# Kernel tuning notes

Measured on AMD Instinct MI355X. Metric: run time of the kernel, lower is better.

Reference implementation:

```python
import jax, jax.numpy as jnp
import numpy as np
import math

N = 8192
IN_FEATURES = 512
OUT_FEATURES = 512
BUCKET = 4          # self.bucket -> number of hash buckets
NHASH = 1           # nHashTable hardcoded to 1 in forward
NEG = -9e15         # sentinel used by the original module


def setup_inputs() -> dict:
    key = jax.random.key(0)
    k_in, k_adj, k_rot, k_kw, k_vw = jax.random.split(key, 5)
    inp = jax.random.normal(k_in, (N, IN_FEATURES), dtype=jnp.float32)
    adj = jax.random.randint(k_adj, (N, N), 0, 2, dtype=jnp.int32)
    rotations_rands = jax.random.normal(k_rot, (NHASH, OUT_FEATURES, BUCKET // 2), dtype=jnp.float32)
    # xavier_uniform with gain=1.414 for (in, out) matrices
    limit = 1.414 * math.sqrt(6.0 / (IN_FEATURES + OUT_FEATURES))
    kW = jax.random.uniform(k_kw, (IN_FEATURES, OUT_FEATURES), minval=-limit, maxval=limit, dtype=jnp.float32)
    vW = jax.random.uniform(k_vw, (IN_FEATURES, OUT_FEATURES), minval=-limit, maxval=limit, dtype=jnp.float32)
    return {"input": inp, "adj": adj, "rotations_rands": rotations_rands, "kW": kW, "vW": vW}


def reference(input, adj, rotations_rands, kW, vW):
    kh = input @ kW                      # [N, H]
    vh = input @ vW                      # [N, H]
    H = kh.shape[1]

    # LSH bucketing: rotate keys, argmax over [r, -r] -> bucket id per node
    rv = jnp.einsum('nh,thb->tnb', kh, rotations_rands)   # [1, N, B/2]
    rv = jnp.concatenate([rv, -rv], axis=-1)              # [1, N, B]
    buckets = jnp.argmax(rv, axis=2)[0]                   # [N]

    # Original scatters per-bucket kh@kh.T blocks into a dense NxN matrix
    # initialized at NEG; equivalent to masking full scores by same-bucket.
    same_bucket = buckets[:, None] == buckets[None, :]    # [N, N]
    scores = (kh @ kh.T) / jnp.sqrt(jnp.asarray(H, kh.dtype))
    K = jnp.where(same_bucket, scores, NEG)

    attention = jnp.where(adj > 0, K, NEG)
    attention = jax.nn.softmax(attention, axis=1)
    # dropout is identity in eval mode (reference runs in eval)
    h_prime = attention @ vh                              # [N, H]
    return jax.nn.elu(h_prime)                            # concat=True -> ELU
```

## Files before the change

kernel.cpp:

```cpp
#include <hip/hip_runtime.h>
#include <hip/hip_bf16.h>
#include <math.h>

#define N_NODES 8192
#define FEAT 512
#define NEGV -9e15f
#define VHPT_W 8704

typedef __attribute__((ext_vector_type(8))) short short8;
typedef __attribute__((ext_vector_type(4))) float floatx4;

#define OFF_VHP   16777216UL
#define OFF_KHP   33554432UL
#define OFF_VHPT  42074112UL
#define OFF_MASK  50987008UL
#define OFF_S     59375616UL
#define OFF_PERM  109707264UL
#define OFF_BUCK  109772800UL
#define OFF_META  109805568UL
#define OFF_CMEAN 109806592UL
#define OFF_ROWI  109841408UL
#define OFF_IPERM 109874176UL
#define WS_NEEDED 109906944UL
#define CAP_S     25165824L

#define OFF_AB    (OFF_S)
#define OFF_WKT   (OFF_S + 16777216UL)
#define OFF_WVT   (OFF_S + 17825792UL)
#define OFF_CW    (OFF_MASK)

static __device__ __forceinline__ unsigned short f2bf_bits(float x) {
  __hip_bfloat16 h = __float2bfloat16(x);
  unsigned short u;
  __builtin_memcpy(&u, &h, 2);
  return u;
}
static __device__ __forceinline__ float bf_bits2f(unsigned short u) {
  __hip_bfloat16 h;
  __builtin_memcpy(&h, &u, 2);
  return __bfloat162float(h);
}

static __device__ __forceinline__ void async_copy16(const void* gptr,
                                                    void* lptr) {
  __builtin_amdgcn_global_load_lds(
      (const __attribute__((address_space(1))) unsigned int*)gptr,
      (__attribute__((address_space(3))) unsigned int*)lptr, 16, 0, 0);
}

__global__ __launch_bounds__(256) void convert_input(
    const float* __restrict__ A, __hip_bfloat16* __restrict__ Ab) {
  const long idx = ((long)blockIdx.x * 256 + threadIdx.x) * 8;
  const float4 v0 = *(const float4*)&A[idx];
  const float4 v1 = *(const float4*)&A[idx + 4];
  const float vv[8] = {v0.x, v0.y, v0.z, v0.w, v1.x, v1.y, v1.z, v1.w};
  union { short8 s; unsigned short u[8]; } o;
#pragma unroll
  for (int e = 0; e < 8; e++) o.u[e] = f2bf_bits(vv[e]);
  *(short8*)&Ab[idx] = o.s;
}

__global__ __launch_bounds__(256) void convert_w(
    const float* __restrict__ kW, const float* __restrict__ vW,
    __hip_bfloat16* __restrict__ WkT, __hip_bfloat16* __restrict__ WvT) {
  __shared__ float tile[64][65];
  const int z = blockIdx.z;
  const float* __restrict__ W = z ? vW : kW;
  __hip_bfloat16* __restrict__ T = z ? WvT : WkT;
  const int k0 = blockIdx.x * 64, n0 = blockIdx.y * 64;
  const int t = threadIdx.x;
#pragma unroll
  for (int s = 0; s < 16; s++) {
    int idx = t + s * 256;
    int r = idx >> 6, c = idx & 63;
    tile[r][c] = W[(long)(k0 + r) * FEAT + n0 + c];
  }
  __syncthreads();
#pragma unroll
  for (int s = 0; s < 16; s++) {
    int idx = t + s * 256;
    int a = idx >> 6, b = idx & 63;
    unsigned short h = f2bf_bits(tile[b][a]);
    __builtin_memcpy(&T[(long)(n0 + a) * FEAT + k0 + b], &h, 2);
  }
}

__global__ __launch_bounds__(256) void mfma_dual(
    const __hip_bfloat16* __restrict__ Ab, const __hip_bfloat16* __restrict__ WkT,
    const __hip_bfloat16* __restrict__ WvT, const int* __restrict__ iperm,
    const int* __restrict__ meta, __hip_bfloat16* __restrict__ khp,
    __hip_bfloat16* __restrict__ vhp) {
  const int z = blockIdx.z;
  const __hip_bfloat16* __restrict__ WT = z ? WvT : WkT;
  const int ti = blockIdx.x, tj = blockIdx.y;
  __shared__ __align__(16) __hip_bfloat16 smem[32768];
  __hip_bfloat16* As = smem;
  __hip_bfloat16* Ws = smem + 16384;
  const int t = threadIdx.x;
  const int lane = t & 63, w = t >> 6;
  const int wm = (w >> 1) * 64, wn = (w & 1) * 64;
  const int quad = lane >> 4, ln = lane & 15;
  const int qr = quad * 8;
  floatx4 acc[4][4];
#pragma unroll
  for (int mi = 0; mi < 4; mi++)
#pragma unroll
    for (int ni = 0; ni < 4; ni++) acc[mi][ni] = (floatx4)0.f;

  auto STAGE = [&](int st, int buf) {
    const int k0 = st * 64;
#pragma unroll
    for (int p = 0; p < 2; p++)
#pragma unroll
      for (int s = 0; s < 2; s++) {
        int c = t + s * 256;
        int row = c >> 2, off8 = (c & 3) * 8;
        int lo = buf * 8192 + p * 4096 + row * 32 + off8;
        async_copy16(&Ab[(long)(ti * 128 + row) * FEAT + k0 + p * 32 + off8],
                     &As[lo]);
        async_copy16(&WT[(long)(tj * 128 + row) * FEAT + k0 + p * 32 + off8],
                     &Ws[lo]);
      }
  };
  STAGE(0, 0);
  __syncthreads();
  for (int st = 0; st < 8; st++) {
    const int buf = st & 1;
    if (st < 7) STAGE(st + 1, buf ^ 1);
#pragma unroll
    for (int p = 0; p < 2; p++) {
      short8 af[4], bfr[4];
#pragma unroll
      for (int mi = 0; mi < 4; mi++)
        af[mi] = *(const short8*)&As[buf * 8192 + p * 4096 +
                                     (wm + mi * 16 + ln) * 32 + qr];
#pragma unroll
      for (int ni = 0; ni < 4; ni++)
        bfr[ni] = *(const short8*)&Ws[buf * 8192 + p * 4096 +
                                      (wn + ni * 16 + ln) * 32 + qr];
#pragma unroll
      for (int mi = 0; mi < 4; mi++)
#pragma unroll
        for (int ni = 0; ni < 4; ni++)
          acc[mi][ni] = __builtin_amdgcn_mfma_f32_16x16x32_bf16(
              af[mi], bfr[ni], acc[mi][ni], 0, 0, 0);
    }
    __syncthreads();
  }
  __hip_bfloat16* Ct = smem;
#pragma unroll
  for (int mi = 0; mi < 4; mi++)
#pragma unroll
    for (int ni = 0; ni < 4; ni++) {
      int col = wn + ni * 16 + ln;
#pragma unroll
      for (int reg = 0; reg < 4; reg++) {
        int row = wm + mi * 16 + quad * 4 + reg;
        Ct[row * 136 + col] = __float2bfloat16(acc[mi][ni][reg]);
      }
    }
  __syncthreads();
  __hip_bfloat16* __restrict__ dst = z ? vhp : khp;
#pragma unroll
  for (int i = 0; i < 8; i++) {
    int idx = t + i * 256;
    int rl = idx >> 4, c8 = (idx & 15) * 8;
    int g = iperm[ti * 128 + rl];
    long drow = g;
    if (z) {
      int bb = (g >= meta[1]) + (g >= meta[2]) + (g >= meta[3]);
      drow = meta[14 + bb] + g - meta[bb];
    }
    *(short8*)&dst[drow * FEAT + tj * 128 + c8] =
        *(const short8*)&Ct[rl * 136 + c8];
  }
}

__global__ __launch_bounds__(64) void cw_kernel(
    const float* __restrict__ kW, const float* __restrict__ rot,
    double* __restrict__ cw) {
  const int f = blockIdx.x;
  const int lane = threadIdx.x;
  double r0 = 0.0, r1 = 0.0;
  for (int h = lane; h < FEAT; h += 64) {
    double a = (double)kW[(long)f * FEAT + h];
    r0 += a * (double)rot[2 * h];
    r1 += a * (double)rot[2 * h + 1];
  }
#pragma unroll
  for (int off = 32; off > 0; off >>= 1) {
    r0 += __shfl_down(r0, off);
    r1 += __shfl_down(r1, off);
  }
  if (lane == 0) {
    cw[2 * f] = r0;
    cw[2 * f + 1] = r1;
  }
}

__global__ __launch_bounds__(64) void rv_bucket_kernel(
    const float* __restrict__ input, const double* __restrict__ cw,
    int* __restrict__ buckets) {
  const int i = blockIdx.x;
  const int lane = threadIdx.x;
  double r0 = 0.0, r1 = 0.0;
  for (int f = lane; f < FEAT; f += 64) {
    double a = (double)input[(long)i * FEAT + f];
    r0 += a * cw[2 * f];
    r1 += a * cw[2 * f + 1];
  }
#pragma unroll
  for (int off = 32; off > 0; off >>= 1) {
    r0 += __shfl_down(r0, off);
    r1 += __shfl_down(r1, off);
  }
  if (lane == 0) {
    int b = 0;
    double best = r0;
    if (r1 > best)  { best = r1;  b = 1; }
    if (-r0 > best) { best = -r0; b = 2; }
    if (-r1 > best) { best = -r1; b = 3; }
    buckets[i] = b;
  }
}

__global__ __launch_bounds__(256) void sort_kernel(
    const int* __restrict__ buckets, int* __restrict__ perm,
    int* __restrict__ iperm, int* __restrict__ meta,
    float* __restrict__ cmean, float* __restrict__ rowsum) {
  __shared__ int lc[4][256];
  __shared__ int sc[4][256];
  __shared__ int boff_sh[5];
  const int t = threadIdx.x;
  cmean[t] = 0.f;
  cmean[t + 256] = 0.f;
  for (int k = t; k < N_NODES; k += 256) rowsum[k] = 0.f;
  const int base = t * 32;
  int c0 = 0, c1 = 0, c2 = 0, c3 = 0;
  for (int k = 0; k < 32; k++) {
    int b = buckets[base + k];
    c0 += (b == 0); c1 += (b == 1); c2 += (b == 2); c3 += (b == 3);
  }
  lc[0][t] = c0; lc[1][t] = c1; lc[2][t] = c2; lc[3][t] = c3;
  sc[0][t] = c0; sc[1][t] = c1; sc[2][t] = c2; sc[3][t] = c3;
  __syncthreads();
  for (int off = 1; off < 256; off <<= 1) {
    int a0 = (t >= off) ? sc[0][t - off] : 0;
    int a1 = (t >= off) ? sc[1][t - off] : 0;
    int a2 = (t >= off) ? sc[2][t - off] : 0;
    int a3 = (t >= off) ? sc[3][t - off] : 0;
    __syncthreads();
    sc[0][t] += a0; sc[1][t] += a1; sc[2][t] += a2; sc[3][t] += a3;
    __syncthreads();
  }
  if (t == 0) {
    int boff[5];
    boff[0] = 0;
    for (int b = 0; b < 4; b++) boff[b + 1] = boff[b] + sc[b][255];
    for (int b = 0; b < 5; b++) { meta[b] = boff[b]; boff_sh[b] = boff[b]; }
    long so = 0;
    int po = 0;
    for (int b = 0; b < 4; b++) {
      int tot = boff[b + 1] - boff[b];
      int pad = ((tot + 127) >> 7) << 7;
      meta[5 + b] = pad;
      meta[9 + b] = (int)so;
      meta[14 + b] = po;
      so += (long)pad * pad;
      po += pad;
    }
    meta[13] = (int)so;
    meta[18] = po;
    if (so > CAP_S)
      for (int b = 0; b < 4; b++) meta[5 + b] = 0;
  }
  __syncthreads();
  int s0 = boff_sh[0] + sc[0][t] - lc[0][t];
  int s1 = boff_sh[1] + sc[1][t] - lc[1][t];
  int s2 = boff_sh[2] + sc[2][t] - lc[2][t];
  int s3 = boff_sh[3] + sc[3][t] - lc[3][t];
  for (int k = 0; k < 32; k++) {
    int i = base + k;
    int b = buckets[i];
    int pos = (b == 0) ? s0++ : ((b == 1) ? s1++ : ((b == 2) ? s2++ : s3++));
    perm[pos] = i;
    iperm[i] = pos;
  }
}

__global__ __launch_bounds__(256) void transpose_vhpT_kernel(
    const __hip_bfloat16* __restrict__ vhp, __hip_bfloat16* __restrict__ vhpT,
    float* __restrict__ cmean) {
  __shared__ float tile[64][65];
  __shared__ float cred[4][64];
  const int g0 = blockIdx.x * 64;
  const int f0 = blockIdx.y * 64;
  const int t = threadIdx.x;
#pragma unroll
  for (int s = 0; s < 4; s++) {
    int idx = t + s * 256;
    int r = idx >> 4, c4 = (idx & 15) * 4;
    ushort4 v = *(const ushort4*)&vhp[(long)(g0 + r) * FEAT + f0 + c4];
    tile[r][c4]     = bf_bits2f(v.x);
    tile[r][c4 + 1] = bf_bits2f(v.y);
    tile[r][c4 + 2] = bf_bits2f(v.z);
    tile[r][c4 + 3] = bf_bits2f(v.w);
  }
  __syncthreads();
  {
    const int c = t & 63, seg = t >> 6;
    float ps = 0.f;
#pragma unroll
    for (int rr = 0; rr < 16; rr++) ps += tile[seg * 16 + rr][c];
    cred[seg][c] = ps;
  }
  __syncthreads();
  if (t < 64)
    atomicAdd(&cmean[f0 + t],
              cred[0][t] + cred[1][t] + cred[2][t] + cred[3][t]);
#pragma unroll
  for (int s = 0; s < 2; s++) {
    int idx = t + s * 256;
    int fr = idx >> 3, gc8 = (idx & 7) * 8;
    union { short8 v; unsigned short u[8]; } pk;
#pragma unroll
    for (int e = 0; e < 8; e++) pk.u[e] = f2bf_bits(tile[gc8 + e][fr]);
    *(short8*)&vhpT[(long)(f0 + fr) * VHPT_W + g0 + gc8] = pk.v;
  }
}

__global__ __launch_bounds__(256) void maskpack_kernel(
    const int* __restrict__ adj, const int* __restrict__ perm,
    const int* __restrict__ meta, unsigned long long* __restrict__ maskbits) {
  __shared__ int adj_lds[N_NODES];
  const int g = blockIdx.x;
  const int t = threadIdx.x;
  const int b = (g >= meta[1]) + (g >= meta[2]) + (g >= meta[3]);
  const int boff = meta[b];
  const int n_b = meta[b + 1] - boff;
  const int padded = meta[5 + b];
  const int i = perm[g];
  const int* arow = adj + (long)i * N_NODES;
#pragma unroll
  for (int s = 0; s < 8; s++) {
    int idx = (t + s * 256) * 4;
    *(int4*)&adj_lds[idx] = *(const int4*)&arow[idx];
  }
  __syncthreads();
  const int lane = t & 63, w = t >> 6;
  for (int jj0 = w * 64; jj0 < padded; jj0 += 256) {
    int jj = jj0 + lane;
    int pred = 0;
    if (jj < n_b) pred = adj_lds[perm[boff + jj]] > 0;
    unsigned long long mword = __ballot(pred);
    if (lane == 0) maskbits[(long)g * 128 + (jj0 >> 6)] = mword;
  }
}

__global__ __launch_bounds__(256) void s_gemm(
    const __hip_bfloat16* __restrict__ khp, const int* __restrict__ meta,
    const unsigned long long* __restrict__ maskbits,
    __hip_bfloat16* __restrict__ S, float* __restrict__ rowsum) {
  const int b = blockIdx.z;
  const int padded = meta[5 + b];
  const int T = padded >> 7;
  const int pairs = (T * (T + 1)) >> 1;
  int L = blockIdx.x;
  if (L >= pairs) return;
  int ti = 0;
  while (L >= T - ti) { L -= T - ti; ti++; }
  const int tj = ti + L;
  const int boff = meta[b];
  const int n_b = meta[b + 1] - boff;
  const long soff = meta[9 + b];
  __shared__ __align__(16) __hip_bfloat16 smem[32768];
  __hip_bfloat16* As = smem;
  __hip_bfloat16* Bs = smem + 16384;
  const int t = threadIdx.x;
  const int lane = t & 63, w = t >> 6;
  const int wm = (w >> 1) * 64, wn = (w & 1) * 64;
  const int quad = lane >> 4, ln = lane & 15;
  const int qr = quad * 8;
  floatx4 acc[4][4];
#pragma unroll
  for (int mi = 0; mi < 4; mi++)
#pragma unroll
    for (int ni = 0; ni < 4; ni++) acc[mi][ni] = (floatx4)0.f;
  const long a_g0 = boff + ti * 128;
  const long b_g0 = boff + tj * 128;

  auto STAGE = [&](int st, int buf) {
    const int k0 = st * 64;
#pragma unroll
    for (int p = 0; p < 2; p++)
#pragma unroll
      for (int s = 0; s < 2; s++) {
        int c = t + s * 256;
        int row = c >> 2, off8 = (c & 3) * 8;
        int lo = buf * 8192 + p * 4096 + row * 32 + off8;
        async_copy16(&khp[(a_g0 + row) * FEAT + k0 + p * 32 + off8], &As[lo]);
        async_copy16(&khp[(b_g0 + row) * FEAT + k0 + p * 32 + off8], &Bs[lo]);
      }
  };
  STAGE(0, 0);
  __syncthreads();
  for (int st = 0; st < 8; st++) {
    const int buf = st & 1;
    if (st < 7) STAGE(st + 1, buf ^ 1);
#pragma unroll
    for (int p = 0; p < 2; p++) {
      short8 af[4], bfr[4];
#pragma unroll
      for (int mi = 0; mi < 4; mi++)
        af[mi] = *(const short8*)&As[buf * 8192 + p * 4096 +
                                     (wm + mi * 16 + ln) * 32 + qr];
#pragma unroll
      for (int ni = 0; ni < 4; ni++)
        bfr[ni] = *(const short8*)&Bs[buf * 8192 + p * 4096 +
                                      (wn + ni * 16 + ln) * 32 + qr];
#pragma unroll
      for (int mi = 0; mi < 4; mi++)
#pragma unroll
        for (int ni = 0; ni < 4; ni++)
          acc[mi][ni] = __builtin_amdgcn_mfma_f32_16x16x32_bf16(
              af[mi], bfr[ni], acc[mi][ni], 0, 0, 0);
    }
    __syncthreads();
  }
  const float scale = 0.04419417382415922f;
  __hip_bfloat16* Ct = smem;
#pragma unroll
  for (int mi = 0; mi < 4; mi++)
#pragma unroll
    for (int ni = 0; ni < 4; ni++) {
      int col = wn + ni * 16 + ln;
#pragma unroll
      for (int reg = 0; reg < 4; reg++) {
        int row = wm + mi * 16 + quad * 4 + reg;
        Ct[row * 136 + col] =
            __float2bfloat16(__expf(acc[mi][ni][reg] * scale));
      }
    }
  __syncthreads();
#pragma unroll
  for (int i = 0; i < 8; i++) {
    int idx = t + i * 256;
    int rl = idx >> 4, c8 = (idx & 15) * 8;
    int rg = ti * 128 + rl;
    int cg = tj * 128 + c8;
    union { short8 v; unsigned short u[8]; } pk;
    pk.v = *(const short8*)&Ct[rl * 136 + c8];
    unsigned long long wbits = maskbits[(long)(boff + rg) * 128 + (cg >> 6)];
    float ps = 0.f;
#pragma unroll
    for (int e = 0; e < 8; e++) {
      if (!((wbits >> ((cg & 63) + e)) & 1ULL)) pk.u[e] = 0;
      ps += bf_bits2f(pk.u[e]);
    }
    *(short8*)&S[soff + (long)rg * padded + cg] = pk.v;
#pragma unroll
    for (int off = 1; off < 16; off <<= 1) ps += __shfl_xor(ps, off);
    if (rg < n_b && (lane & 15) == 0)
      atomicAdd(&rowsum[boff + rg], ps);
  }
  if (ti != tj) {
#pragma unroll
    for (int i = 0; i < 8; i++) {
      int idx = t + i * 256;
      int cl = idx >> 4, r8 = (idx & 15) * 8;
      int rg = tj * 128 + cl;
      int cg = ti * 128 + r8;
      union { short8 v; unsigned short u[8]; } pk;
#pragma unroll
      for (int e = 0; e < 8; e++) {
        __hip_bfloat16 hv = Ct[(r8 + e) * 136 + cl];
        __builtin_memcpy(&pk.u[e], &hv, 2);
      }
      unsigned long long wbits = maskbits[(long)(boff + rg) * 128 + (cg >> 6)];
      float ps = 0.f;
#pragma unroll
      for (int e = 0; e < 8; e++) {
        if (!((wbits >> ((cg & 63) + e)) & 1ULL)) pk.u[e] = 0;
        ps += bf_bits2f(pk.u[e]);
      }
      *(short8*)&S[soff + (long)rg * padded + cg] = pk.v;
#pragma unroll
      for (int off = 1; off < 16; off <<= 1) ps += __shfl_xor(ps, off);
      if (rg < n_b && (lane & 15) == 0)
        atomicAdd(&rowsum[boff + rg], ps);
    }
  }
}

__global__ __launch_bounds__(256) void pv_gemm(
    const __hip_bfloat16* __restrict__ S, const __hip_bfloat16* __restrict__ vhpT,
    const int* __restrict__ meta, const int* __restrict__ perm,
    const float* __restrict__ cmean, const float* __restrict__ rowsum,
    float* __restrict__ out) {
  const int b = blockIdx.z;
  const int padded = meta[5 + b];
  const int ti = blockIdx.x;
  if (ti * 128 >= padded) return;
  const int boff = meta[b];
  const int n_b = meta[b + 1] - boff;
  const long soff = meta[9 + b];
  const int poff = meta[14 + b];
  const int f0 = blockIdx.y * 128;
  __shared__ __align__(16) __hip_bfloat16 As[16384];
  __shared__ __align__(16) __hip_bfloat16 Bs[16384];
  const int t = threadIdx.x;
  const int lane = t & 63, w = t >> 6;
  const int wm = (w >> 1) * 64, wn = (w & 1) * 64;
  const int quad = lane >> 4, ln = lane & 15;
  const int qr = quad * 8;
  floatx4 acc[4][4];
#pragma unroll
  for (int mi = 0; mi < 4; mi++)
#pragma unroll
    for (int ni = 0; ni < 4; ni++) acc[mi][ni] = (floatx4)0.f;
  const long r0 = (long)ti * 128;

  auto STAGE = [&](int st, int buf) {
    const int k0 = st * 64;
#pragma unroll
    for (int p = 0; p < 2; p++)
#pragma unroll
      for (int s = 0; s < 2; s++) {
        int c = t + s * 256;
        int row = c >> 2, off8 = (c & 3) * 8;
        int lo = buf * 8192 + p * 4096 + row * 32 + off8;
        async_copy16(&S[soff + (r0 + row) * padded + k0 + p * 32 + off8],
                     &As[lo]);
        async_copy16(
            &vhpT[(long)(f0 + row) * VHPT_W + poff + k0 + p * 32 + off8],
            &Bs[lo]);
      }
  };
  const int NS = padded >> 6;
  STAGE(0, 0);
  __syncthreads();
  for (int st = 0; st < NS; st++) {
    const int buf = st & 1;
    if (st + 1 < NS) STAGE(st + 1, buf ^ 1);
#pragma unroll
    for (int p = 0; p < 2; p++) {
      short8 af[4], bfr[4];
#pragma unroll
      for (int mi = 0; mi < 4; mi++)
        af[mi] = *(const short8*)&As[buf * 8192 + p * 4096 +
                                     (wm + mi * 16 + ln) * 32 + qr];
#pragma unroll
      for (int ni = 0; ni < 4; ni++)
        bfr[ni] = *(const short8*)&Bs[buf * 8192 + p * 4096 +
                                      (wn + ni * 16 + ln) * 32 + qr];
#pragma unroll
      for (int mi = 0; mi < 4; mi++)
#pragma unroll
        for (int ni = 0; ni < 4; ni++)
          acc[mi][ni] = __builtin_amdgcn_mfma_f32_16x16x32_bf16(
              af[mi], bfr[ni], acc[mi][ni], 0, 0, 0);
    }
    __syncthreads();
  }
#pragma unroll
  for (int mi = 0; mi < 4; mi++) {
#pragma unroll
    for (int reg = 0; reg < 4; reg++) {
      int r = ti * 128 + wm + mi * 16 + quad * 4 + reg;
      if (r < n_b) {
        int g = boff + r;
        int node = perm[g];
        float rs = rowsum[g];
        int fl = (rs == 0.f);
        float inv = fl ? 0.f : 1.f / rs;
#pragma unroll
        for (int ni = 0; ni < 4; ni++) {
          int fc = f0 + wn + ni * 16 + ln;
          float v = fl ? cmean[fc] * (1.f / (float)N_NODES)
                       : acc[mi][ni][reg] * inv;
          v = v > 0.f ? v : expm1f(v);
          out[(long)node * FEAT + fc] = v;
        }
      }
    }
  }
}

__global__ __launch_bounds__(256) void gemm_dual(
    const float* __restrict__ A, const float* __restrict__ Wk,
    const float* __restrict__ Wv, float* __restrict__ kh,
    float* __restrict__ vh) {
  __shared__ float As[32][33];
  __shared__ float Bk[32][33];
  __shared__ float Bv[32][33];
  const int tid = threadIdx.x;
  const int row0 = blockIdx.x * 32;
  const int col0 = blockIdx.y * 32;
  const int tx = tid & 15, ty = tid >> 4;
  float ck00 = 0.f, ck01 = 0.f, ck10 = 0.f, ck11 = 0.f;
  float cv00 = 0.f, cv01 = 0.f, cv10 = 0.f, cv11 = 0.f;
  for (int kt = 0; kt < FEAT; kt += 32) {
#pragma unroll
    for (int t = 0; t < 4; t++) {
      int e = tid + t * 256;
      int r = e >> 5, c = e & 31;
      As[r][c] = A[(long)(row0 + r) * FEAT + kt + c];
      Bk[r][c] = Wk[(long)(kt + r) * FEAT + col0 + c];
      Bv[r][c] = Wv[(long)(kt + r) * FEAT + col0 + c];
    }
    __syncthreads();
#pragma unroll
    for (int kk = 0; kk < 32; kk++) {
      float a0 = As[ty * 2][kk], a1 = As[ty * 2 + 1][kk];
      float bk0 = Bk[kk][tx * 2], bk1 = Bk[kk][tx * 2 + 1];
      float bv0 = Bv[kk][tx * 2], bv1 = Bv[kk][tx * 2 + 1];
      ck00 += a0 * bk0; ck01 += a0 * bk1;
      ck10 += a1 * bk0; ck11 += a1 * bk1;
      cv00 += a0 * bv0; cv01 += a0 * bv1;
      cv10 += a1 * bv0; cv11 += a1 * bv1;
    }
    __syncthreads();
  }
  const int r0 = row0 + ty * 2, c0 = col0 + tx * 2;
  kh[(long)r0 * FEAT + c0] = ck00;       kh[(long)r0 * FEAT + c0 + 1] = ck01;
  kh[(long)(r0 + 1) * FEAT + c0] = ck10; kh[(long)(r0 + 1) * FEAT + c0 + 1] = ck11;
  vh[(long)r0 * FEAT + c0] = cv00;       vh[(long)r0 * FEAT + c0 + 1] = cv01;
  vh[(long)(r0 + 1) * FEAT + c0] = cv10; vh[(long)(r0 + 1) * FEAT + c0 + 1] = cv11;
}

__global__ __launch_bounds__(64) void bucket_kernel(
    const float* __restrict__ kh, const float* __restrict__ rot,
    int* __restrict__ buckets) {
  const int i = blockIdx.x;
  const int lane = threadIdx.x;
  double r0 = 0.0, r1 = 0.0;
  for (int h = lane; h < FEAT; h += 64) {
    double a = (double)kh[(long)i * FEAT + h];
    r0 += a * (double)rot[2 * h];
    r1 += a * (double)rot[2 * h + 1];
  }
#pragma unroll
  for (int off = 32; off > 0; off >>= 1) {
    r0 += __shfl_down(r0, off);
    r1 += __shfl_down(r1, off);
  }
  if (lane == 0) {
    int b = 0;
    double best = r0;
    if (r1 > best)  { best = r1;  b = 1; }
    if (-r0 > best) { best = -r0; b = 2; }
    if (-r1 > best) { best = -r1; b = 3; }
    buckets[i] = b;
  }
}

__global__ __launch_bounds__(256) void attn_kernel(
    const float* __restrict__ kh, const float* __restrict__ vh,
    const int* __restrict__ adj, const int* __restrict__ buckets,
    float* __restrict__ out) {
  __shared__ float khi[FEAT];
  __shared__ float pbuf[N_NODES];
  __shared__ unsigned short jlist[N_NODES];
  __shared__ int cnt_sh;
  __shared__ float red[256];
  const int i = blockIdx.x;
  const int tid = threadIdx.x;
  if (tid == 0) cnt_sh = 0;
  for (int k = tid; k < FEAT; k += 256) khi[k] = kh[(long)i * FEAT + k];
  const int mybucket = buckets[i];
  __syncthreads();
  const int* adjrow = adj + (long)i * N_NODES;
  for (int j = tid; j < N_NODES; j += 256) {
    if (adjrow[j] > 0 && buckets[j] == mybucket) {
      int idx = atomicAdd(&cnt_sh, 1);
      jlist[idx] = (unsigned short)j;
    }
  }
  __syncthreads();
  const int cnt = cnt_sh;
  float mloc = -INFINITY;
  for (int idx = tid; idx < cnt; idx += 256) {
    int j = jlist[idx];
    const float4* kj = (const float4*)(kh + (long)j * FEAT);
    const float4* ki = (const float4*)khi;
    float acc = 0.f;
#pragma unroll 8
    for (int k = 0; k < FEAT / 4; k++) {
      float4 a = ki[k];
      float4 b = kj[k];
      acc += a.x * b.x + a.y * b.y + a.z * b.z + a.w * b.w;
    }
    float s = acc * 0.04419417382415922f;
    pbuf[idx] = s;
    mloc = fmaxf(mloc, s);
  }
  red[tid] = mloc;
  __syncthreads();
#pragma unroll
  for (int off = 128; off > 0; off >>= 1) {
    if (tid < off) red[tid] = fmaxf(red[tid], red[tid + off]);
    __syncthreads();
  }
  const float m = red[0];
  __syncthreads();
  float lloc = 0.f;
  for (int idx = tid; idx < cnt; idx += 256) {
    float p = expf(pbuf[idx] - m);
    pbuf[idx] = p;
    lloc += p;
  }
  red[tid] = lloc;
  __syncthreads();
#pragma unroll
  for (int off = 128; off > 0; off >>= 1) {
    if (tid < off) red[tid] += red[tid + off];
    __syncthreads();
  }
  const float l = red[0];
  __syncthreads();
  const int f = 2 * tid;
  float acc0 = 0.f, acc1 = 0.f;
  if (cnt > 0) {
#pragma unroll 4
    for (int idx = 0; idx < cnt; idx++) {
      int j = jlist[idx];
      float p = pbuf[idx];
      float2 v = *(const float2*)(vh + (long)j * FEAT + f);
      acc0 += p * v.x;
      acc1 += p * v.y;
    }
    float invl = 1.f / l;
    acc0 *= invl;
    acc1 *= invl;
  } else {
    for (int j = 0; j < N_NODES; j++) {
      float2 v = *(const float2*)(vh + (long)j * FEAT + f);
      acc0 += v.x;
      acc1 += v.y;
    }
    acc0 *= (1.f / (float)N_NODES);
    acc1 *= (1.f / (float)N_NODES);
  }
  acc0 = acc0 > 0.f ? acc0 : expm1f(acc0);
  acc1 = acc1 > 0.f ? acc1 : expm1f(acc1);
  *(float2*)(out + (long)i * FEAT + f) = make_float2(acc0, acc1);
}

extern "C" void kernel_launch(void* const* d_in, const int* in_sizes, int n_in,
                              void* d_out, int out_size, void* d_ws,
                              size_t ws_size, hipStream_t stream) {
  const float* input = (const float*)d_in[0];
  const int* adj = (const int*)d_in[1];
  const float* rot = (const float*)d_in[2];
  const float* kW = (const float*)d_in[3];
  const float* vW = (const float*)d_in[4];
  float* out = (float*)d_out;

  char* ws = (char*)d_ws;

  if (ws_size >= WS_NEEDED) {
    __hip_bfloat16* vhp = (__hip_bfloat16*)(ws + OFF_VHP);
    __hip_bfloat16* khp = (__hip_bfloat16*)(ws + OFF_KHP);
    __hip_bfloat16* vhpT = (__hip_bfloat16*)(ws + OFF_VHPT);
    unsigned long long* maskbits = (unsigned long long*)(ws + OFF_MASK);
    __hip_bfloat16* S = (__hip_bfloat16*)(ws + OFF_S);
    int* perm = (int*)(ws + OFF_PERM);
    int* iperm = (int*)(ws + OFF_IPERM);
    int* buckets = (int*)(ws + OFF_BUCK);
    int* meta = (int*)(ws + OFF_META);
    float* cmean = (float*)(ws + OFF_CMEAN);
    float* rowsum = (float*)(ws + OFF_ROWI);
    __hip_bfloat16* Ab = (__hip_bfloat16*)(ws + OFF_AB);
    __hip_bfloat16* WkT = (__hip_bfloat16*)(ws + OFF_WKT);
    __hip_bfloat16* WvT = (__hip_bfloat16*)(ws + OFF_WVT);
    double* cw = (double*)(ws + OFF_CW);

    hipMemsetAsync(ws + OFF_KHP + (size_t)N_NODES * FEAT * 2, 0,
                   128 * FEAT * 2, stream);
    hipMemsetAsync(ws + OFF_VHP, 0, (size_t)VHPT_W * FEAT * 2, stream);
    cw_kernel<<<512, 64, 0, stream>>>(kW, rot, cw);
    rv_bucket_kernel<<<N_NODES, 64, 0, stream>>>(input, cw, buckets);
    sort_kernel<<<1, 256, 0, stream>>>(buckets, perm, iperm, meta, cmean,
                                       rowsum);
    maskpack_kernel<<<N_NODES, 256, 0, stream>>>(adj, perm, meta, maskbits);
    convert_input<<<2048, 256, 0, stream>>>(input, Ab);
    convert_w<<<dim3(8, 8, 2), 256, 0, stream>>>(kW, vW, WkT, WvT);
    mfma_dual<<<dim3(64, 4, 2), 256, 0, stream>>>(Ab, WkT, WvT, iperm, meta,
                                                  khp, vhp);
    transpose_vhpT_kernel<<<dim3(VHPT_W / 64, FEAT / 64), 256, 0, stream>>>(
        vhp, vhpT, cmean);
    s_gemm<<<dim3(2080, 1, 4), 256, 0, stream>>>(khp, meta, maskbits, S,
                                                 rowsum);
    pv_gemm<<<dim3(66, 4, 4), 256, 0, stream>>>(S, vhpT, meta, perm, cmean,
                                                rowsum, out);
  } else {
    float* kh = (float*)(ws + 0UL);
    float* vh = (float*)(ws + 16777216UL);
    int* buckets = (int*)(ws + 33554432UL);
    dim3 gemm_grid(N_NODES / 32, FEAT / 32);
    gemm_dual<<<gemm_grid, 256, 0, stream>>>(input, kW, vW, kh, vh);
    bucket_kernel<<<N_NODES, 64, 0, stream>>>(kh, rot, buckets);
    attn_kernel<<<N_NODES, 256, 0, stream>>>(kh, vh, adj, buckets, out);
  }
}
```

Measured before the change: 552.0 us.

## Bit-pack adjacency up front and shrink pv_gemm row tile for more blocks

Adds a pass that packs each adjacency row into 128 64-bit words, so the permuted mask-pack kernel gathers bits from a small shared array instead of staging a full 32KB int row in LDS. It also halves pv_gemm's row tile to 64 and doubles its grid, giving more workgroups across the CUs. This adds an extra kernel launch and 8MB of workspace writes. The smaller tile lowers per-block data reuse of the vhpT operand.

```diff
diff --git a/kernel.cpp b/kernel.cpp
--- a/kernel.cpp
+++ b/kernel.cpp
@@ -10,6 +10,7 @@
 typedef __attribute__((ext_vector_type(8))) short short8;
 typedef __attribute__((ext_vector_type(4))) float floatx4;
 
+#define OFF_ABITS 0UL
 #define OFF_VHP   16777216UL
 #define OFF_KHP   33554432UL
 #define OFF_VHPT  42074112UL
@@ -46,6 +47,49 @@
   __builtin_amdgcn_global_load_lds(
       (const __attribute__((address_space(1))) unsigned int*)gptr,
       (__attribute__((address_space(3))) unsigned int*)lptr, 16, 0, 0);
+}
+
+__global__ __launch_bounds__(256) void adjbits_kernel(
+    const int* __restrict__ adj, unsigned long long* __restrict__ adjbits) {
+  const int i = blockIdx.x;
+  const int t = threadIdx.x;
+  const int lane = t & 63, w = t >> 6;
+  const int* arow = adj + (long)i * N_NODES;
+  unsigned long long* brow = adjbits + (long)i * 128;
+#pragma unroll
+  for (int s = 0; s < 32; s++) {
+    int col = w * 64 + lane + s * 256;
+    int pred = arow[col] > 0;
+    unsigned long long mword = __ballot(pred);
+    if (lane == 0) brow[s * 4 + w] = mword;
+  }
+}
+
+__global__ __launch_bounds__(256) void maskpack2_kernel(
+    const unsigned long long* __restrict__ adjbits,
+    const int* __restrict__ perm, const int* __restrict__ meta,
+    unsigned long long* __restrict__ maskbits) {
+  __shared__ unsigned long long bits[128];
+  const int g = blockIdx.x;
+  const int t = threadIdx.x;
+  const int b = (g >= meta[1]) + (g >= meta[2]) + (g >= meta[3]);
+  const int boff = meta[b];
+  const int n_b = meta[b + 1] - boff;
+  const int padded = meta[5 + b];
+  const int i = perm[g];
+  if (t < 128) bits[t] = adjbits[(long)i * 128 + t];
+  __syncthreads();
+  const int lane = t & 63, w = t >> 6;
+  for (int jj0 = w * 64; jj0 < padded; jj0 += 256) {
+    int jj = jj0 + lane;
+    int pred = 0;
+    if (jj < n_b) {
+      int p = perm[boff + jj];
+      pred = (int)((bits[p >> 6] >> (p & 63)) & 1ULL);
+    }
+    unsigned long long mword = __ballot(pred);
+    if (lane == 0) maskbits[(long)g * 128 + (jj0 >> 6)] = mword;
+  }
 }
 
 __global__ __launch_bounds__(256) void convert_input(
@@ -326,34 +370,6 @@
 #pragma unroll
     for (int e = 0; e < 8; e++) pk.u[e] = f2bf_bits(tile[gc8 + e][fr]);
     *(short8*)&vhpT[(long)(f0 + fr) * VHPT_W + g0 + gc8] = pk.v;
-  }
-}
-
-__global__ __launch_bounds__(256) void maskpack_kernel(
-    const int* __restrict__ adj, const int* __restrict__ perm,
-    const int* __restrict__ meta, unsigned long long* __restrict__ maskbits) {
-  __shared__ int adj_lds[N_NODES];
-  const int g = blockIdx.x;
-  const int t = threadIdx.x;
-  const int b = (g >= meta[1]) + (g >= meta[2]) + (g >= meta[3]);
-  const int boff = meta[b];
-  const int n_b = meta[b + 1] - boff;
-  const int padded = meta[5 + b];
-  const int i = perm[g];
-  const int* arow = adj + (long)i * N_NODES;
-#pragma unroll
-  for (int s = 0; s < 8; s++) {
-    int idx = (t + s * 256) * 4;
-    *(int4*)&adj_lds[idx] = *(const int4*)&arow[idx];
-  }
-  __syncthreads();
-  const int lane = t & 63, w = t >> 6;
-  for (int jj0 = w * 64; jj0 < padded; jj0 += 256) {
-    int jj = jj0 + lane;
-    int pred = 0;
-    if (jj < n_b) pred = adj_lds[perm[boff + jj]] > 0;
-    unsigned long long mword = __ballot(pred);
-    if (lane == 0) maskbits[(long)g * 128 + (jj0 >> 6)] = mword;
   }
 }
 
@@ -500,41 +516,44 @@
   const int b = blockIdx.z;
   const int padded = meta[5 + b];
   const int ti = blockIdx.x;
-  if (ti * 128 >= padded) return;
+  if (ti * 64 >= padded) return;
   const int boff = meta[b];
   const int n_b = meta[b + 1] - boff;
   const long soff = meta[9 + b];
   const int poff = meta[14 + b];
   const int f0 = blockIdx.y * 128;
-  __shared__ __align__(16) __hip_bfloat16 As[16384];
-  __shared__ __align__(16) __hip_bfloat16 Bs[16384];
+  __shared__ __align__(16) __hip_bfloat16 As[2 * 2 * 2048];
+  __shared__ __align__(16) __hip_bfloat16 Bs[2 * 2 * 4096];
   const int t = threadIdx.x;
   const int lane = t & 63, w = t >> 6;
-  const int wm = (w >> 1) * 64, wn = (w & 1) * 64;
+  const int wm = (w >> 1) * 32, wn = (w & 1) * 64;
   const int quad = lane >> 4, ln = lane & 15;
   const int qr = quad * 8;
-  floatx4 acc[4][4];
-#pragma unroll
-  for (int mi = 0; mi < 4; mi++)
+  floatx4 acc[2][4];
+#pragma unroll
+  for (int mi = 0; mi < 2; mi++)
 #pragma unroll
     for (int ni = 0; ni < 4; ni++) acc[mi][ni] = (floatx4)0.f;
-  const long r0 = (long)ti * 128;
+  const long r0 = (long)ti * 64;
 
   auto STAGE = [&](int st, int buf) {
     const int k0 = st * 64;
 #pragma unroll
-    for (int p = 0; p < 2; p++)
+    for (int p = 0; p < 2; p++) {
+      {
+        int row = t >> 2, off8 = (t & 3) * 8;
+        async_copy16(&S[soff + (r0 + row) * padded + k0 + p * 32 + off8],
+                     &As[buf * 4096 + p * 2048 + row * 32 + off8]);
+      }
 #pragma unroll
       for (int s = 0; s < 2; s++) {
         int c = t + s * 256;
         int row = c >> 2, off8 = (c & 3) * 8;
-        int lo = buf * 8192 + p * 4096 + row * 32 + off8;
-        async_copy16(&S[soff + (r0 + row) * padded + k0 + p * 32 + off8],
-                     &As[lo]);
         async_copy16(
             &vhpT[(long)(f0 + row) * VHPT_W + poff + k0 + p * 32 + off8],
-            &Bs[lo]);
+            &Bs[buf * 8192 + p * 4096 + row * 32 + off8]);
       }
+    }
   };
   const int NS = padded >> 6;
   STAGE(0, 0);
@@ -544,17 +563,17 @@
     if (st + 1 < NS) STAGE(st + 1, buf ^ 1);
 #pragma unroll
     for (int p = 0; p < 2; p++) {
-      short8 af[4], bfr[4];
-#pragma unroll
-      for (int mi = 0; mi < 4; mi++)
-        af[mi] = *(const short8*)&As[buf * 8192 + p * 4096 +
+      short8 af[2], bfr[4];
+#pragma unroll
+      for (int mi = 0; mi < 2; mi++)
+        af[mi] = *(const short8*)&As[buf * 4096 + p * 2048 +
                                      (wm + mi * 16 + ln) * 32 + qr];
 #pragma unroll
       for (int ni = 0; ni < 4; ni++)
         bfr[ni] = *(const short8*)&Bs[buf * 8192 + p * 4096 +
                                       (wn + ni * 16 + ln) * 32 + qr];
 #pragma unroll
-      for (int mi = 0; mi < 4; mi++)
+      for (int mi = 0; mi < 2; mi++)
 #pragma unroll
         for (int ni = 0; ni < 4; ni++)
           acc[mi][ni] = __builtin_amdgcn_mfma_f32_16x16x32_bf16(
@@ -563,10 +582,10 @@
     __syncthreads();
   }
 #pragma unroll
-  for (int mi = 0; mi < 4; mi++) {
+  for (int mi = 0; mi < 2; mi++) {
 #pragma unroll
     for (int reg = 0; reg < 4; reg++) {
-      int r = ti * 128 + wm + mi * 16 + quad * 4 + reg;
+      int r = ti * 64 + wm + mi * 16 + quad * 4 + reg;
       if (r < n_b) {
         int g = boff + r;
         int node = perm[g];
@@ -759,6 +778,7 @@
   char* ws = (char*)d_ws;
 
   if (ws_size >= WS_NEEDED) {
+    unsigned long long* adjbits = (unsigned long long*)(ws + OFF_ABITS);
     __hip_bfloat16* vhp = (__hip_bfloat16*)(ws + OFF_VHP);
     __hip_bfloat16* khp = (__hip_bfloat16*)(ws + OFF_KHP);
     __hip_bfloat16* vhpT = (__hip_bfloat16*)(ws + OFF_VHPT);
@@ -778,11 +798,13 @@
     hipMemsetAsync(ws + OFF_KHP + (size_t)N_NODES * FEAT * 2, 0,
                    128 * FEAT * 2, stream);
     hipMemsetAsync(ws + OFF_VHP, 0, (size_t)VHPT_W * FEAT * 2, stream);
+    adjbits_kernel<<<N_NODES, 256, 0, stream>>>(adj, adjbits);
     cw_kernel<<<512, 64, 0, stream>>>(kW, rot, cw);
     rv_bucket_kernel<<<N_NODES, 64, 0, stream>>>(input, cw, buckets);
     sort_kernel<<<1, 256, 0, stream>>>(buckets, perm, iperm, meta, cmean,
                                        rowsum);
-    maskpack_kernel<<<N_NODES, 256, 0, stream>>>(adj, perm, meta, maskbits);
+    maskpack2_kernel<<<N_NODES, 256, 0, stream>>>(adjbits, perm, meta,
+                                                  maskbits);
     convert_input<<<2048, 256, 0, stream>>>(input, Ab);
     convert_w<<<dim3(8, 8, 2), 256, 0, stream>>>(kW, vW, WkT, WvT);
     mfma_dual<<<dim3(64, 4, 2), 256, 0, stream>>>(Ab, WkT, WvT, iperm, meta,
@@ -791,8 +813,8 @@
         vhp, vhpT, cmean);
     s_gemm<<<dim3(2080, 1, 4), 256, 0, stream>>>(khp, meta, maskbits, S,
                                                  rowsum);
-    pv_gemm<<<dim3(66, 4, 4), 256, 0, stream>>>(S, vhpT, meta, perm, cmean,
-                                                rowsum, out);
+    pv_gemm<<<dim3(128, 4, 4), 256, 0, stream>>>(S, vhpT, meta, perm, cmean,
+                                                 rowsum, out);
   } else {
     float* kh = (float*)(ws + 0UL);
     float* vh = (float*)(ws + 16777216UL);
```

After: 568.8 us. 1.03x slower.
